# Performance work log

Measured on AMD Instinct MI355X. Metric: run time of the kernel, lower is better.

The kernel has to match this reference:

```python
import jax, jax.numpy as jnp
import numpy as np

B, N, E, D_IN, D_H = 32, 20000, 320000, 128, 128


def setup_inputs() -> dict:
    key = jax.random.key(0)
    k1, k2, k3, k4 = jax.random.split(key, 4)
    gene_emb = jax.random.normal(k1, (B, N, D_IN), dtype=jnp.float32)
    edge_index = jax.random.randint(k2, (2, E), 0, N, dtype=jnp.int32)
    # Glorot-ish init for the two GCN linear layers
    W1 = jax.random.normal(k3, (D_IN, D_H), dtype=jnp.float32) / np.sqrt(D_IN)
    b1 = jnp.zeros((D_H,), dtype=jnp.float32)
    W2 = jax.random.normal(k4, (D_H, D_H), dtype=jnp.float32) / np.sqrt(D_H)
    b2 = jnp.zeros((D_H,), dtype=jnp.float32)
    return {"gene_emb": gene_emb, "edge_index": edge_index,
            "W1": W1, "b1": b1, "W2": W2, "b2": b2}


def _gcn_norm(edge_index, num_nodes):
    # PyG GCNConv default: add self-loops, symmetric D^-1/2 (A+I) D^-1/2
    src, dst = edge_index[0], edge_index[1]
    deg = jax.ops.segment_sum(jnp.ones_like(src, dtype=jnp.float32), dst,
                              num_segments=num_nodes) + 1.0  # +1 for self-loop
    dinv = jax.lax.rsqrt(deg)
    edge_norm = dinv[src] * dinv[dst]   # [E]
    self_norm = 1.0 / deg               # dinv[i]*dinv[i]
    return src, dst, edge_norm, self_norm


def _gcn_conv(x, W, b, src, dst, edge_norm, self_norm, num_nodes):
    # x: [B, N, d_in] -> [B, N, d_out]; same graph shared across batch
    h = jnp.einsum('bnd,df->bnf', x, W)
    agg = jax.vmap(lambda hb: jax.ops.segment_sum(
        hb[src] * edge_norm[:, None], dst, num_segments=num_nodes))(h)
    return agg + self_norm[None, :, None] * h + b


def reference(gene_emb, edge_index, W1, b1, W2, b2):
    src, dst, edge_norm, self_norm = _gcn_norm(edge_index, N)
    x = jax.nn.relu(_gcn_conv(gene_emb, W1, b1, src, dst, edge_norm, self_norm, N))
    x = _gcn_conv(x, W2, b2, src, dst, edge_norm, self_norm, N)
    # global_mean_pool over each cloned graph == mean over the node axis
    return jnp.mean(x, axis=1)  # [B, D_H]
```

## Files before the change

### kernel.cpp

```cpp
#include <hip/hip_runtime.h>
#include <stdint.h>

#define N_NODES 20000
#define N_EDGES 320000
#define N_BATCH 32
#define DIM     128

typedef short v8s __attribute__((ext_vector_type(8)));
typedef float v4f __attribute__((ext_vector_type(4)));

static inline int cdiv(int a, int b){ return (a + b - 1) / b; }

__device__ __forceinline__ float bf_lo(uint32_t u){ return __uint_as_float(u << 16); }
__device__ __forceinline__ float bf_hi(uint32_t u){ return __uint_as_float(u & 0xffff0000u); }
__device__ __forceinline__ uint32_t f2bf(float f){
  uint32_t x = __float_as_uint(f);
  return (x + 0x7fffu + ((x >> 16) & 1u)) >> 16;
}
__device__ __forceinline__ uint32_t packbf2(float a, float b){ return f2bf(a) | (f2bf(b) << 16); }
__device__ __forceinline__ uint32_t cvtpk_bf16(float lo, float hi){
  uint32_t r;
  asm volatile("v_cvt_pk_bf16_f32 %0, %1, %2" : "=v"(r) : "v"(lo), "v"(hi));
  return r;
}


__global__ void k_zero(uint32_t* p, int n){
  int i = blockIdx.x * 256 + threadIdx.x;
  if (i < n) p[i] = 0u;
}

__global__ void k_hist(const int* __restrict__ ei, uint32_t* __restrict__ hist){
  int e = blockIdx.x * 256 + threadIdx.x;
  if (e < N_EDGES){
    int d = ei[N_EDGES + e];
    atomicAdd(&hist[d], 1u);
  }
}

__global__ void k_scan(const uint32_t* __restrict__ hist, uint32_t* __restrict__ row_start,
                       float* __restrict__ dinv, float* __restrict__ cw){
  __shared__ uint32_t part[1024];
  const int t = threadIdx.x;
  const int base = t * 20;
  uint32_t cnt[20];
  uint32_t s = 0;
  #pragma unroll
  for (int i = 0; i < 20; i++){
    int idx = base + i;
    uint32_t v = (idx < N_NODES) ? hist[idx] : 0u;
    cnt[i] = v; s += v;
  }
  part[t] = s;
  __syncthreads();
  for (int off = 1; off < 1024; off <<= 1){
    uint32_t v = part[t];
    uint32_t add = (t >= off) ? part[t - off] : 0u;
    __syncthreads();
    part[t] = v + add;
    __syncthreads();
  }
  uint32_t run = (t > 0) ? part[t - 1] : 0u;
  #pragma unroll
  for (int i = 0; i < 20; i++){
    int idx = base + i;
    if (idx < N_NODES){
      row_start[idx] = run;
      float deg = (float)cnt[i] + 1.0f;
      dinv[idx] = rsqrtf(deg);
      cw[idx]   = 1.0f / deg;
      run += cnt[i];
    }
  }
}

__global__ void k_edge(const int* __restrict__ ei, const uint32_t* __restrict__ row_start,
                       uint32_t* __restrict__ cursor, const float* __restrict__ dinv,
                       float* __restrict__ cw, int2* __restrict__ emeta){
  int e = blockIdx.x * 256 + threadIdx.x;
  if (e >= N_EDGES) return;
  int s = ei[e];
  int d = ei[N_EDGES + e];
  float w = dinv[s] * dinv[d];
  atomicAdd(&cw[s], w);
  uint32_t off = atomicAdd(&cursor[d], 1u);
  uint32_t pos = row_start[d] + off;
  emeta[pos] = make_int2(s << 8, __float_as_int(w));
}

__global__ void k_w1pack(const float* __restrict__ W1, uint16_t* __restrict__ W1P){
  int i = blockIdx.x * 256 + threadIdx.x;
  if (i >= 16 * 128 * 8) return;
  int e = i & 7, f = (i >> 3) & 127, q = i >> 10;
  int k = q * 8 + e;
  W1P[i] = (uint16_t)f2bf(W1[k * 128 + f]);
}

__global__ void k_cvt(const float2* __restrict__ x, uint32_t* __restrict__ xb, int n_u32){
  int i = blockIdx.x * 256 + threadIdx.x;
  int stride = gridDim.x * 256;
  for (; i < n_u32; i += stride){
    float2 v = x[i];
    xb[i] = packbf2(v.x, v.y);
  }
}

__global__ __launch_bounds__(256) void k_agg(const uint32_t* __restrict__ xb, uint32_t* __restrict__ yb,
                      const int2* __restrict__ emeta, const uint32_t* __restrict__ row_start,
                      const uint32_t* __restrict__ hist, const float* __restrict__ dinv){
  const int wv = threadIdx.x >> 6, lane = threadIdx.x & 63;
  const int g = lane >> 4, s = lane & 15;
  int n = blockIdx.x * 4 + wv;
  if (n >= N_NODES) return;
  const uint32_t bl = blockIdx.y;
  const char* xbase = (const char*)xb + (size_t)bl * ((size_t)N_NODES * 256);
  const uint32_t s16 = (uint32_t)s * 16u;

  float alo0=0.f, ahi0=0.f, alo1=0.f, ahi1=0.f;
  float alo2=0.f, ahi2=0.f, alo3=0.f, ahi3=0.f;

#define CONS(VV, WW) do { \
    alo0 = fmaf((WW), bf_lo((VV).x), alo0); ahi0 = fmaf((WW), bf_hi((VV).x), ahi0); \
    alo1 = fmaf((WW), bf_lo((VV).y), alo1); ahi1 = fmaf((WW), bf_hi((VV).y), ahi1); \
    alo2 = fmaf((WW), bf_lo((VV).z), alo2); ahi2 = fmaf((WW), bf_hi((VV).z), ahi2); \
    alo3 = fmaf((WW), bf_lo((VV).w), alo3); ahi3 = fmaf((WW), bf_hi((VV).w), ahi3); \
  } while(0)

#define PREP(P, VV, WW) do { \
    uint32_t idx_ = sbase + (P)*4u + (uint32_t)g; \
    uint32_t ci_  = (idx_ < lim) ? idx_ : (lim - 1u); \
    uint32_t so_  = (uint32_t)__shfl(mx, (int)ci_); \
    float    wf_  = __int_as_float(__shfl(my, (int)ci_)); \
    WW = (idx_ < lim) ? wf_ : 0.0f; \
    VV = *reinterpret_cast<const uint4*>(xbase + (so_ + s16)); \
  } while(0)

  float di = dinv[n];
  {
    uint4 sv = *reinterpret_cast<const uint4*>(xbase + ((uint32_t)n * 256u + s16));
    float wself = di * di * 0.25f;
    CONS(sv, wself);
  }

  uint32_t rs  = (uint32_t)__builtin_amdgcn_readfirstlane((int)row_start[n]);
  uint32_t cnt = (uint32_t)__builtin_amdgcn_readfirstlane((int)hist[n]);

  for (uint32_t cbase = 0; cbase < cnt; cbase += 64u){
    uint32_t lim = cnt - cbase; if (lim > 64u) lim = 64u;
    uint32_t cl = (uint32_t)lane; if (cl >= lim) cl = lim - 1u;
    int2 m = emeta[rs + cbase + cl];
    int mx = m.x, my = m.y;

    uint32_t sbase = 0;
    while (sbase + 16u <= lim){
      uint4 p0, p1, p2, p3; float q0, q1, q2, q3;
      PREP(0, p0, q0); PREP(1, p1, q1); PREP(2, p2, q2); PREP(3, p3, q3);
      CONS(p0, q0); CONS(p1, q1); CONS(p2, q2); CONS(p3, q3);
      sbase += 16u;
    }
    if (sbase < lim){
      uint32_t live = lim - sbase;
      uint4 p0, p1, p2, p3; float q0, q1, q2, q3;
      PREP(0, p0, q0);
      if (live > 4u)  { PREP(1, p1, q1); }
      if (live > 8u)  { PREP(2, p2, q2); }
      if (live > 12u) { PREP(3, p3, q3); }
      CONS(p0, q0);
      if (live > 4u)  { CONS(p1, q1); }
      if (live > 8u)  { CONS(p2, q2); }
      if (live > 12u) { CONS(p3, q3); }
    }
  }
#undef PREP
#undef CONS

  alo0 += __shfl_xor(alo0, 16); alo0 += __shfl_xor(alo0, 32);
  ahi0 += __shfl_xor(ahi0, 16); ahi0 += __shfl_xor(ahi0, 32);
  alo1 += __shfl_xor(alo1, 16); alo1 += __shfl_xor(alo1, 32);
  ahi1 += __shfl_xor(ahi1, 16); ahi1 += __shfl_xor(ahi1, 32);
  alo2 += __shfl_xor(alo2, 16); alo2 += __shfl_xor(alo2, 32);
  ahi2 += __shfl_xor(ahi2, 16); ahi2 += __shfl_xor(ahi2, 32);
  alo3 += __shfl_xor(alo3, 16); alo3 += __shfl_xor(alo3, 32);
  ahi3 += __shfl_xor(ahi3, 16); ahi3 += __shfl_xor(ahi3, 32);

  if (lane < 16){
    uint4 o;
    o.x = cvtpk_bf16(alo0, ahi0);
    o.y = cvtpk_bf16(alo1, ahi1);
    o.z = cvtpk_bf16(alo2, ahi2);
    o.w = cvtpk_bf16(alo3, ahi3);
    char* ybase = (char*)yb + (size_t)bl * ((size_t)N_NODES * 256);
    *reinterpret_cast<uint4*>(ybase + ((uint32_t)n * 256u + s16)) = o;
  }
}

__global__ __launch_bounds__(256) void k_gemm(const uint16_t* __restrict__ y,
                                              const uint16_t* __restrict__ W1P,
                                              const float* __restrict__ b1,
                                              const float* __restrict__ cw,
                                              float* __restrict__ S, int b_global0){
  const int w = threadIdx.x >> 6, lane = threadIdx.x & 63;
  const int l15 = lane & 15, q = lane >> 4;
  const int bl = blockIdx.y;

  v8s bfr[4][8];
  #pragma unroll
  for (int q32 = 0; q32 < 4; q32++)
    #pragma unroll
    for (int ft = 0; ft < 8; ft++)
      bfr[q32][ft] = *reinterpret_cast<const v8s*>(W1P + ((q32 * 4 + q) * 128 + ft * 16 + l15) * 8);

  float b1v[8];
  #pragma unroll
  for (int ft = 0; ft < 8; ft++) b1v[ft] = b1[ft * 16 + l15];

  float sacc[8] = {0.f,0.f,0.f,0.f,0.f,0.f,0.f,0.f};

  const int NT = N_NODES / 16;
  int tile0 = (blockIdx.x * 4 + w) * 8;
  for (int t = 0; t < 8; t++){
    int tile = tile0 + t;
    if (tile >= NT) break;
    int n0 = tile * 16;
    const uint16_t* yrow = y + ((size_t)bl * N_NODES + n0 + l15) * DIM + q * 8;
    v8s a0 = *reinterpret_cast<const v8s*>(yrow);
    v8s a1 = *reinterpret_cast<const v8s*>(yrow + 32);
    v8s a2 = *reinterpret_cast<const v8s*>(yrow + 64);
    v8s a3 = *reinterpret_cast<const v8s*>(yrow + 96);

    v4f acc[8];
    #pragma unroll
    for (int ft = 0; ft < 8; ft++) acc[ft] = (v4f){0.f,0.f,0.f,0.f};
    #pragma unroll
    for (int ft = 0; ft < 8; ft++) acc[ft] = __builtin_amdgcn_mfma_f32_16x16x32_bf16(a0, bfr[0][ft], acc[ft], 0, 0, 0);
    #pragma unroll
    for (int ft = 0; ft < 8; ft++) acc[ft] = __builtin_amdgcn_mfma_f32_16x16x32_bf16(a1, bfr[1][ft], acc[ft], 0, 0, 0);
    #pragma unroll
    for (int ft = 0; ft < 8; ft++) acc[ft] = __builtin_amdgcn_mfma_f32_16x16x32_bf16(a2, bfr[2][ft], acc[ft], 0, 0, 0);
    #pragma unroll
    for (int ft = 0; ft < 8; ft++) acc[ft] = __builtin_amdgcn_mfma_f32_16x16x32_bf16(a3, bfr[3][ft], acc[ft], 0, 0, 0);

    float4 cvv = *reinterpret_cast<const float4*>(cw + n0 + q * 4);
    float cvr[4] = {cvv.x, cvv.y, cvv.z, cvv.w};
    #pragma unroll
    for (int ft = 0; ft < 8; ft++){
      #pragma unroll
      for (int r = 0; r < 4; r++){
        float v = acc[ft][r] + b1v[ft];
        v = fmaxf(v, 0.0f);
        sacc[ft] = fmaf(v, cvr[r], sacc[ft]);
      }
    }
  }

  #pragma unroll
  for (int ft = 0; ft < 8; ft++){
    float v = sacc[ft];
    v += __shfl_xor(v, 16);
    v += __shfl_xor(v, 32);
    if (lane < 16) atomicAdd(&S[(b_global0 + bl) * DIM + ft * 16 + lane], v);
  }
}

__global__ void k_final(const float* __restrict__ S, const float* __restrict__ W2,
                        const float* __restrict__ b2, float* __restrict__ out){
  int i = blockIdx.x * 256 + threadIdx.x;
  if (i >= N_BATCH * DIM) return;
  int b = i >> 7, f = i & 127;
  float o = 0.0f;
  const float invN = 1.0f / (float)N_NODES;
  #pragma unroll 4
  for (int k = 0; k < 128; k++)
    o = fmaf(S[b * 128 + k], W2[k * 128 + f], o);
  out[i] = fmaf(o, invN, b2[f]);
}


extern "C" void kernel_launch(void* const* d_in, const int* in_sizes, int n_in,
                              void* d_out, int out_size, void* d_ws, size_t ws_size,
                              hipStream_t stream){
  const float* gene = (const float*)d_in[0];
  const int*   ei   = (const int*)d_in[1];
  const float* W1   = (const float*)d_in[2];
  const float* b1   = (const float*)d_in[3];
  const float* W2   = (const float*)d_in[4];
  const float* b2   = (const float*)d_in[5];
  float* out = (float*)d_out;

  char* base = (char*)d_ws;
  size_t off = 0;
  auto take = [&](size_t bytes)->char*{
    char* p = base + off;
    off = (off + bytes + 255) & ~(size_t)255;
    return p;
  };

  const int ZWORDS = (N_NODES + 1) + N_NODES + N_BATCH * DIM;
  uint32_t* zzone  = (uint32_t*)take((size_t)ZWORDS * 4);
  uint32_t* hist   = zzone;
  uint32_t* cursor = zzone + (N_NODES + 1);
  float*    S      = (float*)(zzone + (N_NODES + 1) + N_NODES);

  uint32_t* row_start = (uint32_t*)take((size_t)N_NODES * 4);
  float*    dinv      = (float*)take((size_t)N_NODES * 4);
  float*    cw        = (float*)take((size_t)N_NODES * 4);
  int2*     emeta     = (int2*)take((size_t)N_EDGES * 8);
  uint16_t* W1P       = (uint16_t*)take((size_t)16 * 128 * 8 * 2);

  const size_t per_batch = (size_t)N_NODES * DIM * 2;
  size_t remain = (ws_size > off) ? (ws_size - off) : 0;
  int C = (int)(remain / (2 * per_batch));
  if (C < 1) C = 1;
  if (C > N_BATCH) C = N_BATCH;
  uint32_t* xb = (uint32_t*)take(per_batch * C);
  uint32_t* yb = (uint32_t*)take(per_batch * C);

  k_zero<<<cdiv(ZWORDS, 256), 256, 0, stream>>>(zzone, ZWORDS);
  k_hist<<<cdiv(N_EDGES, 256), 256, 0, stream>>>(ei, hist);
  k_scan<<<1, 1024, 0, stream>>>(hist, row_start, dinv, cw);
  k_edge<<<cdiv(N_EDGES, 256), 256, 0, stream>>>(ei, row_start, cursor, dinv, cw, emeta);
  k_w1pack<<<64, 256, 0, stream>>>(W1, W1P);

  for (int b0 = 0; b0 < N_BATCH; b0 += C){
    int Cb = (N_BATCH - b0 < C) ? (N_BATCH - b0) : C;
    int nu = Cb * N_NODES * (DIM / 2);
    k_cvt<<<cdiv(nu, 2048), 256, 0, stream>>>(((const float2*)gene) + (size_t)b0 * N_NODES * (DIM / 2), xb, nu);
    k_agg<<<dim3(N_NODES / 4, Cb), 256, 0, stream>>>(xb, yb, emeta, row_start, hist, dinv);
    k_gemm<<<dim3(cdiv(N_NODES / 16, 32), Cb), 256, 0, stream>>>((const uint16_t*)yb, W1P, b1, cw, S, b0);
  }

  k_final<<<cdiv(N_BATCH * DIM, 256), 256, 0, stream>>>(S, W2, b2, out);
}
```

Before: 508.6 us.

## Switch intermediate storage from bf16 to fp16 with fused mixed-precision FMA

Intermediates move from bf16 to fp16 end to end: the input conversion packs with cvt_pkrtz, the aggregation uses v_fma_mix_f32 to multiply-add fp16 halves straight into fp32 accumulators without unpacking, and the GEMM uses fp16 MFMA. The conversion kernel is also widened to 16-byte loads and stores, with a capped grid. This aims to remove the per-element bf16 unpack ALU work in the gather-heavy aggregation and to make the conversion pass cheaper. Risk: fp16 has a narrower range than bf16, and the conversion rounds toward zero.

```diff
diff --git a/kernel.cpp b/kernel.cpp
--- a/kernel.cpp
+++ b/kernel.cpp
@@ -6,22 +6,22 @@
 #define N_BATCH 32
 #define DIM     128
 
-typedef short v8s __attribute__((ext_vector_type(8)));
+typedef _Float16 v8h __attribute__((ext_vector_type(8)));
 typedef float v4f __attribute__((ext_vector_type(4)));
 
 static inline int cdiv(int a, int b){ return (a + b - 1) / b; }
 
-__device__ __forceinline__ float bf_lo(uint32_t u){ return __uint_as_float(u << 16); }
-__device__ __forceinline__ float bf_hi(uint32_t u){ return __uint_as_float(u & 0xffff0000u); }
-__device__ __forceinline__ uint32_t f2bf(float f){
-  uint32_t x = __float_as_uint(f);
-  return (x + 0x7fffu + ((x >> 16) & 1u)) >> 16;
-}
-__device__ __forceinline__ uint32_t packbf2(float a, float b){ return f2bf(a) | (f2bf(b) << 16); }
-__device__ __forceinline__ uint32_t cvtpk_bf16(float lo, float hi){
-  uint32_t r;
-  asm volatile("v_cvt_pk_bf16_f32 %0, %1, %2" : "=v"(r) : "v"(lo), "v"(hi));
-  return r;
+__device__ __forceinline__ uint32_t pk_f16(float lo, float hi){
+  auto h = __builtin_amdgcn_cvt_pkrtz(lo, hi);
+  return __builtin_bit_cast(uint32_t, h);
+}
+__device__ __forceinline__ void fmix_lo(float& acc, uint32_t u, float w){
+  asm("v_fma_mix_f32 %0, %1, %2, %0 op_sel:[0,0,0] op_sel_hi:[1,0,0]"
+      : "+v"(acc) : "v"(u), "v"(w));
+}
+__device__ __forceinline__ void fmix_hi(float& acc, uint32_t u, float w){
+  asm("v_fma_mix_f32 %0, %1, %2, %0 op_sel:[1,0,0] op_sel_hi:[1,0,0]"
+      : "+v"(acc) : "v"(u), "v"(w));
 }
 
 
@@ -93,15 +93,21 @@
   if (i >= 16 * 128 * 8) return;
   int e = i & 7, f = (i >> 3) & 127, q = i >> 10;
   int k = q * 8 + e;
-  W1P[i] = (uint16_t)f2bf(W1[k * 128 + f]);
-}
-
-__global__ void k_cvt(const float2* __restrict__ x, uint32_t* __restrict__ xb, int n_u32){
+  W1P[i] = (uint16_t)(pk_f16(W1[k * 128 + f], 0.0f) & 0xffffu);
+}
+
+__global__ void k_cvt(const float4* __restrict__ x, uint4* __restrict__ xb, int n_u4){
   int i = blockIdx.x * 256 + threadIdx.x;
   int stride = gridDim.x * 256;
-  for (; i < n_u32; i += stride){
-    float2 v = x[i];
-    xb[i] = packbf2(v.x, v.y);
+  for (; i < n_u4; i += stride){
+    float4 f0 = x[2 * i];
+    float4 f1 = x[2 * i + 1];
+    uint4 o;
+    o.x = pk_f16(f0.x, f0.y);
+    o.y = pk_f16(f0.z, f0.w);
+    o.z = pk_f16(f1.x, f1.y);
+    o.w = pk_f16(f1.z, f1.w);
+    xb[i] = o;
   }
 }
 
@@ -116,14 +122,13 @@
   const char* xbase = (const char*)xb + (size_t)bl * ((size_t)N_NODES * 256);
   const uint32_t s16 = (uint32_t)s * 16u;
 
-  float alo0=0.f, ahi0=0.f, alo1=0.f, ahi1=0.f;
-  float alo2=0.f, ahi2=0.f, alo3=0.f, ahi3=0.f;
+  float a0=0.f, a1=0.f, a2=0.f, a3=0.f, a4=0.f, a5=0.f, a6=0.f, a7=0.f;
 
 #define CONS(VV, WW) do { \
-    alo0 = fmaf((WW), bf_lo((VV).x), alo0); ahi0 = fmaf((WW), bf_hi((VV).x), ahi0); \
-    alo1 = fmaf((WW), bf_lo((VV).y), alo1); ahi1 = fmaf((WW), bf_hi((VV).y), ahi1); \
-    alo2 = fmaf((WW), bf_lo((VV).z), alo2); ahi2 = fmaf((WW), bf_hi((VV).z), ahi2); \
-    alo3 = fmaf((WW), bf_lo((VV).w), alo3); ahi3 = fmaf((WW), bf_hi((VV).w), ahi3); \
+    fmix_lo(a0, (VV).x, (WW)); fmix_hi(a1, (VV).x, (WW)); \
+    fmix_lo(a2, (VV).y, (WW)); fmix_hi(a3, (VV).y, (WW)); \
+    fmix_lo(a4, (VV).z, (WW)); fmix_hi(a5, (VV).z, (WW)); \
+    fmix_lo(a6, (VV).w, (WW)); fmix_hi(a7, (VV).w, (WW)); \
   } while(0)
 
 #define PREP(P, VV, WW) do { \
@@ -174,21 +179,21 @@
 #undef PREP
 #undef CONS
 
-  alo0 += __shfl_xor(alo0, 16); alo0 += __shfl_xor(alo0, 32);
-  ahi0 += __shfl_xor(ahi0, 16); ahi0 += __shfl_xor(ahi0, 32);
-  alo1 += __shfl_xor(alo1, 16); alo1 += __shfl_xor(alo1, 32);
-  ahi1 += __shfl_xor(ahi1, 16); ahi1 += __shfl_xor(ahi1, 32);
-  alo2 += __shfl_xor(alo2, 16); alo2 += __shfl_xor(alo2, 32);
-  ahi2 += __shfl_xor(ahi2, 16); ahi2 += __shfl_xor(ahi2, 32);
-  alo3 += __shfl_xor(alo3, 16); alo3 += __shfl_xor(alo3, 32);
-  ahi3 += __shfl_xor(ahi3, 16); ahi3 += __shfl_xor(ahi3, 32);
+  a0 += __shfl_xor(a0, 16); a0 += __shfl_xor(a0, 32);
+  a1 += __shfl_xor(a1, 16); a1 += __shfl_xor(a1, 32);
+  a2 += __shfl_xor(a2, 16); a2 += __shfl_xor(a2, 32);
+  a3 += __shfl_xor(a3, 16); a3 += __shfl_xor(a3, 32);
+  a4 += __shfl_xor(a4, 16); a4 += __shfl_xor(a4, 32);
+  a5 += __shfl_xor(a5, 16); a5 += __shfl_xor(a5, 32);
+  a6 += __shfl_xor(a6, 16); a6 += __shfl_xor(a6, 32);
+  a7 += __shfl_xor(a7, 16); a7 += __shfl_xor(a7, 32);
 
   if (lane < 16){
     uint4 o;
-    o.x = cvtpk_bf16(alo0, ahi0);
-    o.y = cvtpk_bf16(alo1, ahi1);
-    o.z = cvtpk_bf16(alo2, ahi2);
-    o.w = cvtpk_bf16(alo3, ahi3);
+    o.x = pk_f16(a0, a1);
+    o.y = pk_f16(a2, a3);
+    o.z = pk_f16(a4, a5);
+    o.w = pk_f16(a6, a7);
     char* ybase = (char*)yb + (size_t)bl * ((size_t)N_NODES * 256);
     *reinterpret_cast<uint4*>(ybase + ((uint32_t)n * 256u + s16)) = o;
   }
@@ -203,12 +208,12 @@
   const int l15 = lane & 15, q = lane >> 4;
   const int bl = blockIdx.y;
 
-  v8s bfr[4][8];
+  v8h bfr[4][8];
   #pragma unroll
   for (int q32 = 0; q32 < 4; q32++)
     #pragma unroll
     for (int ft = 0; ft < 8; ft++)
-      bfr[q32][ft] = *reinterpret_cast<const v8s*>(W1P + ((q32 * 4 + q) * 128 + ft * 16 + l15) * 8);
+      bfr[q32][ft] = *reinterpret_cast<const v8h*>(W1P + ((q32 * 4 + q) * 128 + ft * 16 + l15) * 8);
 
   float b1v[8];
   #pragma unroll
@@ -223,22 +228,22 @@
     if (tile >= NT) break;
     int n0 = tile * 16;
     const uint16_t* yrow = y + ((size_t)bl * N_NODES + n0 + l15) * DIM + q * 8;
-    v8s a0 = *reinterpret_cast<const v8s*>(yrow);
-    v8s a1 = *reinterpret_cast<const v8s*>(yrow + 32);
-    v8s a2 = *reinterpret_cast<const v8s*>(yrow + 64);
-    v8s a3 = *reinterpret_cast<const v8s*>(yrow + 96);
+    v8h a0 = *reinterpret_cast<const v8h*>(yrow);
+    v8h a1 = *reinterpret_cast<const v8h*>(yrow + 32);
+    v8h a2 = *reinterpret_cast<const v8h*>(yrow + 64);
+    v8h a3 = *reinterpret_cast<const v8h*>(yrow + 96);
 
     v4f acc[8];
     #pragma unroll
     for (int ft = 0; ft < 8; ft++) acc[ft] = (v4f){0.f,0.f,0.f,0.f};
     #pragma unroll
-    for (int ft = 0; ft < 8; ft++) acc[ft] = __builtin_amdgcn_mfma_f32_16x16x32_bf16(a0, bfr[0][ft], acc[ft], 0, 0, 0);
-    #pragma unroll
-    for (int ft = 0; ft < 8; ft++) acc[ft] = __builtin_amdgcn_mfma_f32_16x16x32_bf16(a1, bfr[1][ft], acc[ft], 0, 0, 0);
-    #pragma unroll
-    for (int ft = 0; ft < 8; ft++) acc[ft] = __builtin_amdgcn_mfma_f32_16x16x32_bf16(a2, bfr[2][ft], acc[ft], 0, 0, 0);
-    #pragma unroll
-    for (int ft = 0; ft < 8; ft++) acc[ft] = __builtin_amdgcn_mfma_f32_16x16x32_bf16(a3, bfr[3][ft], acc[ft], 0, 0, 0);
+    for (int ft = 0; ft < 8; ft++) acc[ft] = __builtin_amdgcn_mfma_f32_16x16x32_f16(a0, bfr[0][ft], acc[ft], 0, 0, 0);
+    #pragma unroll
+    for (int ft = 0; ft < 8; ft++) acc[ft] = __builtin_amdgcn_mfma_f32_16x16x32_f16(a1, bfr[1][ft], acc[ft], 0, 0, 0);
+    #pragma unroll
+    for (int ft = 0; ft < 8; ft++) acc[ft] = __builtin_amdgcn_mfma_f32_16x16x32_f16(a2, bfr[2][ft], acc[ft], 0, 0, 0);
+    #pragma unroll
+    for (int ft = 0; ft < 8; ft++) acc[ft] = __builtin_amdgcn_mfma_f32_16x16x32_f16(a3, bfr[3][ft], acc[ft], 0, 0, 0);
 
     float4 cvv = *reinterpret_cast<const float4*>(cw + n0 + q * 4);
     float cvr[4] = {cvv.x, cvv.y, cvv.z, cvv.w};
@@ -323,8 +328,10 @@
 
   for (int b0 = 0; b0 < N_BATCH; b0 += C){
     int Cb = (N_BATCH - b0 < C) ? (N_BATCH - b0) : C;
-    int nu = Cb * N_NODES * (DIM / 2);
-    k_cvt<<<cdiv(nu, 2048), 256, 0, stream>>>(((const float2*)gene) + (size_t)b0 * N_NODES * (DIM / 2), xb, nu);
+    int nu4 = Cb * N_NODES * (DIM / 8);
+    int cvtb = cdiv(nu4, 256 * 8); if (cvtb > 2048) cvtb = 2048;
+    k_cvt<<<cvtb, 256, 0, stream>>>(((const float4*)gene) + (size_t)b0 * N_NODES * (DIM / 4),
+                                    (uint4*)xb, nu4);
     k_agg<<<dim3(N_NODES / 4, Cb), 256, 0, stream>>>(xb, yb, emeta, row_start, hist, dinv);
     k_gemm<<<dim3(cdiv(N_NODES / 16, 32), Cb), 256, 0, stream>>>((const uint16_t*)yb, W1P, b1, cw, S, b0);
   }
```

After: 493.9 us. -2.9%, faster.
